# Performance work log

Hardware: AMD Instinct MI355X
Metric: run time of the kernel (lower is better)

Reference implementation:

```python
import jax, jax.numpy as jnp
from jax import lax
import numpy as np

B, T, F = 32, 512, 512
NUM_OUTPUTS = 23   # joints
DEV_CLASSES = 8
# layer specs: (input_dim, units)
LAYERS = [(F, 1024), (1024, 128), (128, NUM_OUTPUTS),
          (128 + NUM_OUTPUTS, 256), (256, 128), (128, DEV_CLASSES)]


def _gru_params(key, fan_in, units):
    k1, k2, k3 = jax.random.split(key, 3)
    kernel = jax.random.normal(k1, (fan_in, 3 * units), jnp.float32) / jnp.sqrt(jnp.float32(fan_in))
    rkernel = jax.random.normal(k2, (units, 3 * units), jnp.float32) * jnp.float32(0.02)
    bias = jnp.zeros((2, 3 * units), jnp.float32)  # [input_bias, recurrent_bias] (reset_after=True)
    return kernel, rkernel, bias


def setup_inputs() -> dict:
    key = jax.random.key(0)
    keys = jax.random.split(key, 7)
    inp = {"x": jax.random.normal(keys[0], (B, T, F), jnp.float32)}
    for i, (fi, u) in enumerate(LAYERS):
        k, r, b = _gru_params(keys[i + 1], fi, u)
        inp[f"k{i+1}"] = k
        inp[f"r{i+1}"] = r
        inp[f"b{i+1}"] = b
    return inp


def gru(x, kernel, rkernel, bias, act):
    """Keras GRU, reset_after=True, recurrent_activation=sigmoid, gate order z|r|h.
    x: [B,T,F]; kernel: [F,3U]; rkernel: [U,3U]; bias: [2,3U]. Returns [B,T,U]."""
    units = rkernel.shape[0]
    b_i, b_r = bias[0], bias[1]
    # precompute input projections for all timesteps (one big GEMM)
    xp = jnp.einsum('btf,fg->btg', x, kernel) + b_i  # [B,T,3U]

    def step(h, xt):
        rp = h @ rkernel + b_r                       # [B,3U]
        xz, xr, xh = jnp.split(xt, 3, axis=-1)
        rz, rr, rh = jnp.split(rp, 3, axis=-1)
        z = jax.nn.sigmoid(xz + rz)
        r = jax.nn.sigmoid(xr + rr)
        hh = act(xh + r * rh)                        # reset applied AFTER recurrent matmul
        h_new = z * h + (1.0 - z) * hh
        return h_new, h_new

    h0 = jnp.zeros((x.shape[0], units), x.dtype)
    _, ys = lax.scan(step, h0, jnp.swapaxes(xp, 0, 1))  # scan over time
    return jnp.swapaxes(ys, 0, 1)                        # [B,T,U]


relu = jax.nn.relu
linear = lambda v: v


def reference(x, k1, r1, b1, k2, r2, b2, k3, r3, b3,
              k4, r4, b4, k5, r5, b5, k6, r6, b6):
    z = gru(x, k1, r1, b1, relu)          # tcn_gru1: 1024
    z1 = gru(z, k2, r2, b2, relu)         # tcn_gru2: 128
    ye = gru(z1, k3, r3, b3, linear)      # tcn_dgru: num_outputs
    yc = jnp.concatenate([z1, ye], axis=-1)
    y = gru(yc, k4, r4, b4, relu)         # dev_gru1: 256
    y = gru(y, k5, r5, b5, relu)          # dev_gru2: 128
    yd = gru(y, k6, r6, b6, linear)       # dev_dgru: dev_classes
    return ye, yd
```

## Files before the change

### kernel.cpp

```cpp
#include <hip/hip_runtime.h>
#include <hip/hip_bf16.h>
#include <cstdint>
#include <cstddef>

#define BB 32
#define TT 512

typedef short s8v __attribute__((ext_vector_type(8)));
typedef float f4v __attribute__((ext_vector_type(4)));
typedef unsigned long long u64;
typedef unsigned short u16;
typedef unsigned int u32;

__device__ __forceinline__ short f2b(float x) {
  __hip_bfloat16 h = __float2bfloat16(x);
  return *reinterpret_cast<short*>(&h);
}
__device__ __forceinline__ float b2f(u16 x) {
  __hip_bfloat16 h = *reinterpret_cast<__hip_bfloat16*>(&x);
  return __bfloat162float(h);
}
__device__ __forceinline__ float sigm(float x) { return 1.f / (1.f + __expf(-x)); }

__device__ __forceinline__ f4v load16_sc(const void* p) {
  f4v v;
  asm volatile("global_load_dwordx4 %0, %1, off sc0 sc1" : "=v"(v) : "v"(p));
  return v;
}
__device__ __forceinline__ void vm_wait0() {
  asm volatile("s_waitcnt vmcnt(0)" ::: "memory");
}
__device__ __forceinline__ u32 ldP(const u32* p) {
  return __hip_atomic_load(p, __ATOMIC_RELAXED, __HIP_MEMORY_SCOPE_AGENT);
}
__device__ __forceinline__ void stW(u32* p, u32 v) {
  __hip_atomic_store(p, v, __ATOMIC_RELAXED, __HIP_MEMORY_SCOPE_AGENT);
}
__device__ __forceinline__ u32 ldW(const u32* p) {
  return __hip_atomic_load(p, __ATOMIC_RELAXED, __HIP_MEMORY_SCOPE_AGENT);
}

__device__ __forceinline__ void waitP(u32* flags, int baseA, int na, u32 thA,
                                      int baseB, int nbb, u32 thB,
                                      int baseS, int ns, u32 thS) {
  const int tid = threadIdx.x;
  for (;;) {
    int ok = 1;
    if (tid < na) ok = (ldP(&flags[(baseA + tid) * 32]) >= thA) ? 1 : 0;
    else if (tid < na + nbb) ok = (ldP(&flags[(baseB + tid - na) * 32]) >= thB) ? 1 : 0;
    else if (tid < na + nbb + ns) ok = (ldP(&flags[(baseS + tid - na - nbb) * 32]) >= thS) ? 1 : 0;
    if (__syncthreads_count(ok) == (int)blockDim.x) break;
    __builtin_amdgcn_s_sleep(1);
  }
}

__global__ __launch_bounds__(256) void cast_bf16(const float* __restrict__ in,
                                                 u16* __restrict__ outp, int n4) {
  int i = blockIdx.x * 256 + threadIdx.x;
  if (i < n4) {
    float4 v = *(const float4*)(in + (size_t)i * 4);
    u16 o[4] = {(u16)f2b(v.x), (u16)f2b(v.y), (u16)f2b(v.z), (u16)f2b(v.w)};
    *(u64*)(outp + (size_t)i * 4) = *(const u64*)o;
  }
}

__global__ __launch_bounds__(256) void prep_frags(const float* __restrict__ src,
                                                  u16* __restrict__ dst,
                                                  int N, int Ksrc, int Ks,
                                                  int JT, int U, int recmode, int total_fid) {
  int t = blockIdx.x * 256 + threadIdx.x;
  int lane = t & 63, fid = t >> 6;
  if (fid >= total_fid) return;
  int l15 = lane & 15, quad = lane >> 4;
  int ks = fid % Ks;
  int n, valid_n;
  if (recmode) {
    int rest = fid / Ks;
    int jt = rest % JT;
    int g = rest / JT;
    int jj = jt * 16 + l15;
    n = g * U + jj;
    valid_n = (jj < U) ? 1 : 0;
  } else {
    int nt = fid / Ks;
    n = nt * 16 + l15;
    valid_n = (n < N) ? 1 : 0;
  }
  u16* o = dst + ((size_t)fid * 64 + lane) * 8;
#pragma unroll
  for (int j = 0; j < 8; ++j) {
    int k = ks * 32 + quad * 8 + j;
    float v = (valid_n && k < Ksrc) ? src[(size_t)k * N + n] : 0.f;
    o[j] = (u16)f2b(v);
  }
}

__global__ __launch_bounds__(256) void prep_comb(const float* __restrict__ Kmat,
                                                 const float* __restrict__ Rmat,
                                                 u16* __restrict__ dst,
                                                 int N, int U, int w1v, int w1p,
                                                 int w2v, int w2p, int Ks, int JT,
                                                 int total_fid) {
  int t = blockIdx.x * 256 + threadIdx.x;
  int lane = t & 63, fid = t >> 6;
  if (fid >= total_fid) return;
  int l15 = lane & 15, quad = lane >> 4;
  int ks = fid % Ks;
  int rest = fid / Ks;
  int jt = rest % JT;
  int g = rest / JT;
  int j = jt * 16 + l15;
  bool jv = (j < U);
  int n = g * U + (jv ? j : 0);
  u16* o = dst + ((size_t)fid * 64 + lane) * 8;
#pragma unroll
  for (int jj = 0; jj < 8; ++jj) {
    int k = ks * 32 + quad * 8 + jj;
    float v = 0.f;
    if (jv) {
      if (k < w1p) {
        if (k < w1v) v = Kmat[(size_t)k * N + n];
      } else if (k < w1p + w2p) {
        int kr = k - w1p;
        if (kr < w2v) v = Kmat[(size_t)(w1v + kr) * N + n];
      } else {
        int rr = k - w1p - w2p;
        if (rr < U) v = Rmat[(size_t)rr * N + n];
      }
    }
    o[jj] = (u16)f2b(v);
  }
}

__global__ __launch_bounds__(256) void gemm_mfma(const u16* __restrict__ A, int strideA, int Kact,
                                                 const u16* __restrict__ Bf,
                                                 const float* __restrict__ bias,
                                                 float* __restrict__ C,
                                                 int N, int Ntiles, int Ks,
                                                 int t0, int tcLog2) {
  __shared__ char sha[16 * 2056];
  const int tid = threadIdx.x;
  const int lane = tid & 63, l15 = lane & 15, quad = lane >> 4, w = tid >> 6;
  const int KS4 = Ks * 8;
  const int rowB = Ks * 64 + 8;
  const int bm = blockIdx.y * 16;

  for (int i = tid; i < 16 * KS4; i += 256) {
    int r = i / KS4, u = i - r * KS4;
    u64 v = 0;
    if (u * 4 < Kact) {
      int rl = bm + r;
      size_t grow;
      if (t0 >= 0) {
        int tcm = (1 << tcLog2) - 1;
        grow = (((size_t)(rl >> tcLog2)) << 9) + t0 + (rl & tcm);
      } else {
        grow = (size_t)rl;
      }
      v = *((const u64*)(A + grow * (size_t)strideA) + u);
    }
    *(u64*)(sha + r * rowB + u * 8) = v;
  }
  __syncthreads();

  f4v acc[4];
  f4v z4 = {0.f, 0.f, 0.f, 0.f};
#pragma unroll
  for (int q = 0; q < 4; ++q) acc[q] = z4;

  const int ntb = blockIdx.x * 16 + w * 4;
  for (int ks = 0; ks < Ks; ++ks) {
    int off = l15 * rowB + ks * 64 + quad * 16;
    s8v a = *(const s8v*)(sha + off);
#pragma unroll
    for (int q = 0; q < 4; ++q) {
      int nt = ntb + q;
      if (nt < Ntiles) {
        s8v b = *(const s8v*)(Bf + (((size_t)nt * Ks + ks) * 64 + lane) * 8);
        acc[q] = __builtin_amdgcn_mfma_f32_16x16x32_bf16(a, b, acc[q], 0, 0, 0);
      }
    }
  }
#pragma unroll
  for (int q = 0; q < 4; ++q) {
    int nt = ntb + q;
    if (nt >= Ntiles) continue;
    int col = nt * 16 + l15;
    if (col < N) {
      float bv = bias[col];
#pragma unroll
      for (int r = 0; r < 4; ++r) {
        int rowl = bm + quad * 4 + r;
        C[(size_t)rowl * N + col] = acc[q][r] + bv;
      }
    }
  }
}

struct GCfg {
  const u16 *s1, *s2;
  const u16* Bf;
  const float* bias;
  u16* ydst;
  float* fdst;
  u16* hglob;
  int w1p, w2p, Upad, U, Ks, ksIn, JT, nb, base, act, wfd;
  int baseA, na, baseB, nbb;
};

#define SMEM_BYTES 91648
#define HPOFF 74240

__device__ __attribute__((noinline)) void stage_l1(
    const float* xp, const u16* Bf, const float* brec, u16* hbuf, u16* yout,
    u32* flags, int t0, int tc, char* smem) {
  const int tid = threadIdx.x;
  const int lane = tid & 63, l15 = lane & 15, quad = (lane >> 4) & 3;
  const int w = tid >> 6;
  const int blk = blockIdx.x;
  const bool work = (w < 4);
  const int jt = blk * 4 + (w & 3);
  const int j = jt * 16 + l15;
  const int HP = 32 * 1024;

  const float bz = brec[j], brr = brec[1024 + j], bh = brec[2048 + j];
  float hprev[8];
  if (work) {
    const u32* hp = (const u32*)(hbuf + (size_t)(t0 & 1) * HP);
#pragma unroll
    for (int Mt = 0; Mt < 2; ++Mt)
#pragma unroll
      for (int r = 0; r < 4; ++r) {
        int b = Mt * 16 + quad * 4 + r;
        u32 wd = ldW(hp + ((b * 1024 + (j & ~1)) >> 1));
        hprev[Mt * 4 + r] = b2f((j & 1) ? (u16)(wd >> 16) : (u16)(wd & 0xffff));
      }
  }

  for (int tt = 0; tt < tc; ++tt) {
    const int t = t0 + tt;
    waitP(flags, 0, 16, (u32)t, 0, 0, 0, 0, 0, 0);
    float xv[3][8];
    if (work) {
#pragma unroll
      for (int Mt = 0; Mt < 2; ++Mt)
#pragma unroll
        for (int r = 0; r < 4; ++r) {
          int b = Mt * 16 + quad * 4 + r;
          const float* xr_ = xp + ((size_t)b * tc + tt) * 3072;
          xv[0][Mt * 4 + r] = __builtin_nontemporal_load(xr_ + j);
          xv[1][Mt * 4 + r] = __builtin_nontemporal_load(xr_ + 1024 + j);
          xv[2][Mt * 4 + r] = __builtin_nontemporal_load(xr_ + 2048 + j);
        }
    }
    {
      const char* hsrc = (const char*)(hbuf + (size_t)(t & 1) * HP);
      f4v vals[8];
#pragma unroll
      for (int i = 0; i < 8; ++i)
        vals[i] = load16_sc(hsrc + (size_t)(tid + i * 512) * 16);
      vm_wait0();
#pragma unroll
      for (int i = 0; i < 8; ++i) {
        int g16 = tid + i * 512;
        *(f4v*)(smem + (g16 >> 7) * 2064 + (g16 & 127) * 16) = vals[i];
      }
    }
    __syncthreads();
    f4v acc[3][2];
    f4v z4 = {0.f, 0.f, 0.f, 0.f};
#pragma unroll
    for (int g = 0; g < 3; ++g) { acc[g][0] = z4; acc[g][1] = z4; }
    if (work) {
#pragma unroll 4
      for (int ks = 0; ks < 32; ++ks) {
        s8v a0 = *(const s8v*)(smem + l15 * 2064 + ks * 64 + quad * 16);
        s8v a1 = *(const s8v*)(smem + (16 + l15) * 2064 + ks * 64 + quad * 16);
#pragma unroll
        for (int g = 0; g < 3; ++g) {
          s8v b = *(const s8v*)(Bf + (((size_t)(g * 64 + jt) * 32 + ks) * 64 + lane) * 8);
          acc[g][0] = __builtin_amdgcn_mfma_f32_16x16x32_bf16(a0, b, acc[g][0], 0, 0, 0);
          acc[g][1] = __builtin_amdgcn_mfma_f32_16x16x32_bf16(a1, b, acc[g][1], 0, 0, 0);
        }
      }
      u16* hdst = hbuf + (size_t)((t + 1) & 1) * HP;
#pragma unroll
      for (int Mt = 0; Mt < 2; ++Mt)
#pragma unroll
        for (int r = 0; r < 4; ++r) {
          int b = Mt * 16 + quad * 4 + r;
          size_t row = (size_t)b * tc + tt;
          float z = sigm(xv[0][Mt * 4 + r] + acc[0][Mt][r] + bz);
          float rr = sigm(xv[1][Mt * 4 + r] + acc[1][Mt][r] + brr);
          float hh = fmaxf(xv[2][Mt * 4 + r] + rr * (acc[2][Mt][r] + bh), 0.f);
          float hnew = z * hprev[Mt * 4 + r] + (1.f - z) * hh;
          hprev[Mt * 4 + r] = hnew;
          float part = __shfl_xor(hnew, 1, 64);
          if ((l15 & 1) == 0) {
            u32 wd = (u32)(u16)f2b(hnew) | ((u32)(u16)f2b(part) << 16);
            stW((u32*)hdst + ((b * 1024 + j) >> 1), wd);
            stW((u32*)yout + ((row * 1024 + j) >> 1), wd);
          }
        }
    }
    __syncthreads();
    if (tid == 0) stW(&flags[blk * 32], (u32)(t + 1));
  }
}

__device__ __attribute__((noinline)) void stage_gen(
    const GCfg& c, int bs, u32* flags, int t0, int tc, int initH, char* smem) {
  const int tid = threadIdx.x;
  const int lane = tid & 63, l15 = lane & 15, quad = (lane >> 4) & 3;
  const int w = tid >> 6;
  const int rowA = (c.w1p + c.w2p + c.Upad) * 2 + 16;
  const int rowH = c.Upad * 2 + 16;
  char* Ab = smem;
  char* Hp = smem + HPOFF;
  const int HB = 32 * rowH;
  const int uIn = (c.w1p + c.w2p) >> 3;
  const int uH = c.Upad >> 3;
  const int upr = uIn + ((c.nb > 1) ? uH : 0);
  const int total_units = 32 * upr;
  const int u1 = c.w1p >> 3;
  const int U = c.U;
  const int HPstride = 32 * c.Upad;

  int tjt[2];
  bool tv[2];
#pragma unroll
  for (int i = 0; i < 2; ++i) {
    int jt = (w + i * 8) * c.nb + bs;
    tv[i] = (jt < c.JT);
    tjt[i] = tv[i] ? jt : 0;
  }

  const float* b0 = c.bias;
  const float* b1 = c.bias + 3 * U;
  float bz[2], br_[2], bih[2], brh[2];
  int jl[2];
  bool jv[2];
#pragma unroll
  for (int i = 0; i < 2; ++i) {
    int j = tjt[i] * 16 + l15;
    jv[i] = tv[i] && (j < U);
    int jc = jv[i] ? j : 0;
    jl[i] = j;
    bz[i] = b0[jc] + b1[jc];
    br_[i] = b0[U + jc] + b1[U + jc];
    bih[i] = b0[2 * U + jc];
    brh[i] = b1[2 * U + jc];
  }

  if (c.nb == 1) {
    for (int i = tid; i < (2 * HB) >> 2; i += 512) ((u32*)Hp)[i] = 0;
    __syncthreads();
    if (!initH) {
      for (int i = tid; i < 32 * uH; i += 512) {
        int m = i / uH, u = i - m * uH;
        *(f4v*)(Hp + (t0 & 1) * HB + m * rowH + u * 16) = *((const f4v*)c.hglob + i);
      }
    }
    __syncthreads();
  }

  float hprev[2][8];
#pragma unroll
  for (int i = 0; i < 2; ++i) {
    if (!tv[i]) continue;
#pragma unroll
    for (int Mt = 0; Mt < 2; ++Mt)
#pragma unroll
      for (int r = 0; r < 4; ++r) {
        int b = Mt * 16 + quad * 4 + r;
        float hv;
        if (c.nb > 1) {
          u32 wd = ldW((const u32*)c.hglob + (((t0 & 1) * HPstride + b * c.Upad + (jl[i] & ~1)) >> 1));
          hv = b2f((jl[i] & 1) ? (u16)(wd >> 16) : (u16)(wd & 0xffff));
        } else {
          hv = b2f(*(const u16*)(Hp + (t0 & 1) * HB + b * rowH + jl[i] * 2));
        }
        hprev[i][Mt * 4 + r] = jv[i] ? hv : 0.f;
      }
  }

  for (int tt = 0; tt < tc; ++tt) {
    const int t = t0 + tt;
    waitP(flags, c.baseA, c.na, (u32)(t + 1), c.baseB, c.nbb, (u32)(t + 1),
          c.base, (c.nb > 1) ? c.nb : 0, (u32)t);
    {
      f4v vals[10];
      int offs[10];
#pragma unroll
      for (int i = 0; i < 10; ++i) {
        int idx = tid + i * 512;
        int pidx = (idx < total_units) ? idx : (total_units - 1);
        int m = pidx / upr, u = pidx - m * upr;
        const char* src;
        if (u < u1)
          src = (const char*)c.s1 + ((size_t)(m * tc + tt) * c.w1p + (u << 3)) * 2;
        else if (u < uIn)
          src = (const char*)c.s2 + ((size_t)(m * tc + tt) * c.w2p + ((u - u1) << 3)) * 2;
        else
          src = (const char*)c.hglob + ((size_t)(t & 1) * HPstride + m * c.Upad + ((u - uIn) << 3)) * 2;
        vals[i] = load16_sc(src);
        offs[i] = m * rowA + u * 16;
      }
      vm_wait0();
#pragma unroll
      for (int i = 0; i < 10; ++i)
        if (tid + i * 512 < total_units) *(f4v*)(Ab + offs[i]) = vals[i];
    }
    __syncthreads();
    f4v az[2][2], ar[2][2], axh[2][2], arh[2][2];
    f4v z4 = {0.f, 0.f, 0.f, 0.f};
#pragma unroll
    for (int i = 0; i < 2; ++i)
#pragma unroll
      for (int Mt = 0; Mt < 2; ++Mt) { az[i][Mt] = z4; ar[i][Mt] = z4; axh[i][Mt] = z4; arh[i][Mt] = z4; }
    for (int ks = 0; ks < c.ksIn; ++ks) {
      s8v aM[2];
#pragma unroll
      for (int Mt = 0; Mt < 2; ++Mt)
        aM[Mt] = *(const s8v*)(Ab + (Mt * 16 + l15) * rowA + ks * 64 + quad * 16);
#pragma unroll
      for (int i = 0; i < 2; ++i) {
        if (!tv[i]) break;
        const u16* bb = c.Bf + ((size_t)tjt[i] * c.Ks + ks) * 512 + lane * 8;
        s8v bz_ = *(const s8v*)(bb);
        s8v br2 = *(const s8v*)(bb + (size_t)c.JT * c.Ks * 512);
        s8v bh2 = *(const s8v*)(bb + (size_t)2 * c.JT * c.Ks * 512);
#pragma unroll
        for (int Mt = 0; Mt < 2; ++Mt) {
          az[i][Mt] = __builtin_amdgcn_mfma_f32_16x16x32_bf16(aM[Mt], bz_, az[i][Mt], 0, 0, 0);
          ar[i][Mt] = __builtin_amdgcn_mfma_f32_16x16x32_bf16(aM[Mt], br2, ar[i][Mt], 0, 0, 0);
          axh[i][Mt] = __builtin_amdgcn_mfma_f32_16x16x32_bf16(aM[Mt], bh2, axh[i][Mt], 0, 0, 0);
        }
      }
    }
    for (int ks = c.ksIn; ks < c.Ks; ++ks) {
      s8v aM[2];
#pragma unroll
      for (int Mt = 0; Mt < 2; ++Mt) {
        if (c.nb > 1)
          aM[Mt] = *(const s8v*)(Ab + (Mt * 16 + l15) * rowA + ks * 64 + quad * 16);
        else
          aM[Mt] = *(const s8v*)(Hp + (t & 1) * HB + (Mt * 16 + l15) * rowH + (ks - c.ksIn) * 64 + quad * 16);
      }
#pragma unroll
      for (int i = 0; i < 2; ++i) {
        if (!tv[i]) break;
        const u16* bb = c.Bf + ((size_t)tjt[i] * c.Ks + ks) * 512 + lane * 8;
        s8v bz_ = *(const s8v*)(bb);
        s8v br2 = *(const s8v*)(bb + (size_t)c.JT * c.Ks * 512);
        s8v bh2 = *(const s8v*)(bb + (size_t)2 * c.JT * c.Ks * 512);
#pragma unroll
        for (int Mt = 0; Mt < 2; ++Mt) {
          az[i][Mt] = __builtin_amdgcn_mfma_f32_16x16x32_bf16(aM[Mt], bz_, az[i][Mt], 0, 0, 0);
          ar[i][Mt] = __builtin_amdgcn_mfma_f32_16x16x32_bf16(aM[Mt], br2, ar[i][Mt], 0, 0, 0);
          arh[i][Mt] = __builtin_amdgcn_mfma_f32_16x16x32_bf16(aM[Mt], bh2, arh[i][Mt], 0, 0, 0);
        }
      }
    }
#pragma unroll
    for (int i = 0; i < 2; ++i) {
      if (!tv[i]) break;
#pragma unroll
      for (int Mt = 0; Mt < 2; ++Mt)
#pragma unroll
        for (int r = 0; r < 4; ++r) {
          int b = Mt * 16 + quad * 4 + r;
          size_t row = (size_t)b * tc + tt;
          float z = sigm(az[i][Mt][r] + bz[i]);
          float rg = sigm(ar[i][Mt][r] + br_[i]);
          float hh = axh[i][Mt][r] + bih[i] + rg * (arh[i][Mt][r] + brh[i]);
          if (c.act) hh = fmaxf(hh, 0.f);
          float hnew = z * hprev[i][Mt * 4 + r] + (1.f - z) * hh;
          if (!jv[i]) hnew = 0.f;
          hprev[i][Mt * 4 + r] = hnew;
          int j = jl[i];
          float part = __shfl_xor(hnew, 1, 64);
          u32 wd = (u32)(u16)f2b(hnew) | ((u32)(u16)f2b(part) << 16);
          if ((l15 & 1) == 0) {
            if (c.ydst) stW((u32*)c.ydst + ((row * c.Upad + j) >> 1), wd);
            if (c.nb > 1)
              stW((u32*)c.hglob + ((((t + 1) & 1) * HPstride + b * c.Upad + j) >> 1), wd);
          }
          if (c.nb == 1) *(u16*)(Hp + ((t + 1) & 1) * HB + b * rowH + j * 2) = (u16)f2b(hnew);
          if (c.fdst && jv[i] && j < c.wfd)
            c.fdst[((size_t)b * TT + t) * c.wfd + j] = hnew;
        }
    }
    __syncthreads();
    if (tid == 0) stW(&flags[(c.base + bs) * 32], (u32)(t + 1));
  }
  if (c.nb == 1) {
    int pf = (t0 + tc) & 1;
    for (int i = tid; i < 32 * uH; i += 512) {
      int m = i / uH, u = i - m * uH;
      *((f4v*)c.hglob + i) = *(const f4v*)(Hp + pf * HB + m * rowH + u * 16);
    }
  }
}

__global__ __launch_bounds__(512, 1) void pipeline(
    const float* xp, const u16* BfL1, const float* brecL1, u16* hbufL1, u16* y1c,
    GCfg c1, GCfg c2, GCfg c3, GCfg c4, GCfg c5,
    u32* flags, int t0, int tc, int initH) {
  __shared__ char smem[SMEM_BYTES];
  int blk = blockIdx.x;
  if (blk < 16) stage_l1(xp, BfL1, brecL1, hbufL1, y1c, flags, t0, tc, smem);
  else if (blk < 18) stage_gen(c1, blk - 16, flags, t0, tc, initH, smem);
  else if (blk < 19) stage_gen(c2, 0, flags, t0, tc, initH, smem);
  else if (blk < 21) stage_gen(c3, blk - 19, flags, t0, tc, initH, smem);
  else if (blk < 22) stage_gen(c4, 0, flags, t0, tc, initH, smem);
  else stage_gen(c5, 0, flags, t0, tc, initH, smem);
}

extern "C" void kernel_launch(void* const* d_in, const int* in_sizes, int n_in,
                              void* d_out, int out_size, void* d_ws, size_t ws_size,
                              hipStream_t stream) {
  const float* x = (const float*)d_in[0];

  int tcLog2 = 6;
  {
    size_t fixed = (size_t)16384 * 512 * 2
                   + (3145728ull + 1572864ull + 442368 + 15360 + 319488 + 147456 + 7680) * 2
                   + 300000;
    for (; tcLog2 >= 4; --tcLog2) {
      size_t rc = (size_t)BB << tcLog2;
      size_t per = rc * 3072 * 4 + rc * (1024 + 128 + 32 + 256 + 128) * 2 + 8192;
      if (fixed + per <= ws_size || tcLog2 == 4) break;
    }
  }
  const int Tc = 1 << tcLog2;
  const int NCk = TT / Tc;
  const size_t RC = (size_t)BB * Tc;

  char* ws = (char*)d_ws;
  size_t off = 0;
  auto alloc = [&](size_t bytes) -> char* {
    char* p = ws + off;
    off += (bytes + 255) & ~(size_t)255;
    return p;
  };

  u32* flags = (u32*)alloc(23 * 32 * sizeof(u32));
  u16* hbufL1 = (u16*)alloc((size_t)2 * 32 * 1024 * 2);
  u16* hb2 = (u16*)alloc((size_t)2 * 32 * 128 * 2);
  u16* hb4 = (u16*)alloc((size_t)2 * 32 * 256 * 2);
  u16* hs3 = (u16*)alloc((size_t)32 * 32 * 2);
  u16* hs5 = (u16*)alloc((size_t)32 * 128 * 2);
  u16* hs6 = (u16*)alloc((size_t)32 * 32 * 2);
  u16* recB1 = (u16*)alloc(3145728ull * 2);
  u16* gemB1 = (u16*)alloc(1572864ull * 2);
  u16* cB[5];
  const size_t cBe[5] = {442368, 15360, 319488, 147456, 7680};
  for (int i = 0; i < 5; ++i) cB[i] = (u16*)alloc(cBe[i] * 2);
  u16* x16 = (u16*)alloc((size_t)16384 * 512 * 2);
  float* xp = (float*)alloc(RC * 3072 * sizeof(float));
  u16* y1c = (u16*)alloc(RC * 1024 * 2);
  u16* y2c = (u16*)alloc(RC * 128 * 2);
  u16* yec = (u16*)alloc(RC * 32 * 2);
  u16* y4c = (u16*)alloc(RC * 256 * 2);
  u16* y5c = (u16*)alloc(RC * 128 * 2);

  float* outye = (float*)d_out;
  float* outyd = outye + (size_t)BB * TT * 23;

  hipMemsetAsync(flags, 0, 23 * 32 * sizeof(u32), stream);
  hipMemsetAsync(hbufL1, 0, (size_t)2 * 32 * 1024 * 2, stream);
  hipMemsetAsync(hb2, 0, (size_t)2 * 32 * 128 * 2, stream);
  hipMemsetAsync(hb4, 0, (size_t)2 * 32 * 256 * 2, stream);

  {
    int n4 = (16384 * 512) / 4;
    hipLaunchKernelGGL(cast_bf16, dim3((n4 + 255) / 256), dim3(256), 0, stream, x, x16, n4);
    hipLaunchKernelGGL(prep_frags, dim3((3 * 64 * 32 * 64 + 255) / 256), dim3(256), 0, stream,
                       (const float*)d_in[2], recB1, 3072, 1024, 32, 64, 1024, 1, 3 * 64 * 32);
    hipLaunchKernelGGL(prep_frags, dim3((192 * 16 * 64 + 255) / 256), dim3(256), 0, stream,
                       (const float*)d_in[1], gemB1, 3072, 512, 16, 0, 0, 0, 192 * 16);
    const int pc[5][8] = {
        {384, 128, 1024, 1024, 0, 0, 36, 8},
        {69, 23, 128, 128, 0, 0, 5, 2},
        {768, 256, 128, 128, 23, 32, 13, 16},
        {384, 128, 256, 256, 0, 0, 12, 8},
        {24, 8, 128, 128, 0, 0, 5, 1}};
    for (int i = 0; i < 5; ++i) {
      int l = i + 1;
      int tf = 3 * pc[i][7] * pc[i][6];
      hipLaunchKernelGGL(prep_comb, dim3((tf * 64 + 255) / 256), dim3(256), 0, stream,
                         (const float*)d_in[1 + 3 * l], (const float*)d_in[2 + 3 * l], cB[i],
                         pc[i][0], pc[i][1], pc[i][2], pc[i][3], pc[i][4], pc[i][5],
                         pc[i][6], pc[i][7], tf);
    }
  }

  GCfg c1 = {y1c, nullptr, cB[0], (const float*)d_in[6], y2c, nullptr, hb2,
             1024, 0, 128, 128, 36, 32, 8, 2, 16, 1, 0, 0, 16, 0, 0};
  GCfg c2 = {y2c, nullptr, cB[1], (const float*)d_in[9], yec, outye, hs3,
             128, 0, 32, 23, 5, 4, 2, 1, 18, 0, 23, 16, 2, 0, 0};
  GCfg c3 = {y2c, yec, cB[2], (const float*)d_in[12], y4c, nullptr, hb4,
             128, 32, 256, 256, 13, 5, 16, 2, 19, 1, 0, 16, 2, 18, 1};
  GCfg c4 = {y4c, nullptr, cB[3], (const float*)d_in[15], y5c, nullptr, hs5,
             256, 0, 128, 128, 12, 8, 8, 1, 21, 1, 0, 19, 2, 0, 0};
  GCfg c5 = {y5c, nullptr, cB[4], (const float*)d_in[18], nullptr, outyd, hs6,
             128, 0, 32, 8, 5, 4, 1, 1, 22, 0, 8, 21, 1, 0, 0};

  const float* biasL1 = (const float*)d_in[3];

  for (int c = 0; c < NCk; ++c) {
    const int t0 = c * Tc;
    hipLaunchKernelGGL(gemm_mfma, dim3(12, (unsigned)(RC / 16)), dim3(256), 0, stream,
                       x16, 512, 512, gemB1, biasL1, xp, 3072, 192, 16, t0, tcLog2);
    hipLaunchKernelGGL(pipeline, dim3(23), dim3(512), 0, stream,
                       xp, recB1, biasL1 + 3072, hbufL1, y1c,
                       c1, c2, c3, c4, c5, flags, t0, Tc, (c == 0) ? 1 : 0);
  }
}
```

Before: 16.32 ms.

## Use per-wave flags, double-buffered LDS, and x prefetch in layer-1 GRU

```diff
diff --git a/kernel.cpp b/kernel.cpp
--- a/kernel.cpp
+++ b/kernel.cpp
@@ -40,16 +40,16 @@
   return __hip_atomic_load(p, __ATOMIC_RELAXED, __HIP_MEMORY_SCOPE_AGENT);
 }
 
-__device__ __forceinline__ void waitP(u32* flags, int baseA, int na, u32 thA,
+__device__ __forceinline__ void waitW(u32* flags, int baseA, int na, u32 thA,
                                       int baseB, int nbb, u32 thB,
                                       int baseS, int ns, u32 thS) {
-  const int tid = threadIdx.x;
+  const int lane = threadIdx.x & 63;
   for (;;) {
-    int ok = 1;
-    if (tid < na) ok = (ldP(&flags[(baseA + tid) * 32]) >= thA) ? 1 : 0;
-    else if (tid < na + nbb) ok = (ldP(&flags[(baseB + tid - na) * 32]) >= thB) ? 1 : 0;
-    else if (tid < na + nbb + ns) ok = (ldP(&flags[(baseS + tid - na - nbb) * 32]) >= thS) ? 1 : 0;
-    if (__syncthreads_count(ok) == (int)blockDim.x) break;
+    bool ok = true;
+    if (lane < na) ok = (ldP(&flags[(baseA + lane) * 32]) >= thA);
+    if (nbb && lane < nbb) ok = ok && (ldP(&flags[(baseB + lane) * 32]) >= thB);
+    if (ns && lane < ns) ok = ok && (ldP(&flags[(baseS + lane) * 32]) >= thS);
+    if (__all(ok)) break;
     __builtin_amdgcn_s_sleep(1);
   }
 }
@@ -208,7 +208,8 @@
   int baseA, na, baseB, nbb;
 };
 
-#define SMEM_BYTES 91648
+#define SMEM_BYTES 132096
+#define HBUF1 66048
 #define HPOFF 74240
 
 __device__ __attribute__((noinline)) void stage_l1(
@@ -222,6 +223,7 @@
   const int jt = blk * 4 + (w & 3);
   const int j = jt * 16 + l15;
   const int HP = 32 * 1024;
+  const int slot = blk * 4 + (w & 3);
 
   const float bz = brec[j], brr = brec[1024 + j], bh = brec[2048 + j];
   float hprev[8];
@@ -237,22 +239,24 @@
       }
   }
 
+  float xc[3][8];
+  if (work) {
+#pragma unroll
+    for (int Mt = 0; Mt < 2; ++Mt)
+#pragma unroll
+      for (int r = 0; r < 4; ++r) {
+        int b = Mt * 16 + quad * 4 + r;
+        const float* xr_ = xp + ((size_t)b * tc + 0) * 3072;
+        xc[0][Mt * 4 + r] = __builtin_nontemporal_load(xr_ + j);
+        xc[1][Mt * 4 + r] = __builtin_nontemporal_load(xr_ + 1024 + j);
+        xc[2][Mt * 4 + r] = __builtin_nontemporal_load(xr_ + 2048 + j);
+      }
+  }
+
   for (int tt = 0; tt < tc; ++tt) {
     const int t = t0 + tt;
-    waitP(flags, 0, 16, (u32)t, 0, 0, 0, 0, 0, 0);
-    float xv[3][8];
-    if (work) {
-#pragma unroll
-      for (int Mt = 0; Mt < 2; ++Mt)
-#pragma unroll
-        for (int r = 0; r < 4; ++r) {
-          int b = Mt * 16 + quad * 4 + r;
-          const float* xr_ = xp + ((size_t)b * tc + tt) * 3072;
-          xv[0][Mt * 4 + r] = __builtin_nontemporal_load(xr_ + j);
-          xv[1][Mt * 4 + r] = __builtin_nontemporal_load(xr_ + 1024 + j);
-          xv[2][Mt * 4 + r] = __builtin_nontemporal_load(xr_ + 2048 + j);
-        }
-    }
+    waitW(flags, 0, 64, (u32)t, 0, 0, 0, 0, 0, 0);
+    char* buf = smem + (t & 1) * HBUF1;
     {
       const char* hsrc = (const char*)(hbuf + (size_t)(t & 1) * HP);
       f4v vals[8];
@@ -263,19 +267,33 @@
 #pragma unroll
       for (int i = 0; i < 8; ++i) {
         int g16 = tid + i * 512;
-        *(f4v*)(smem + (g16 >> 7) * 2064 + (g16 & 127) * 16) = vals[i];
+        *(f4v*)(buf + (g16 >> 7) * 2064 + (g16 & 127) * 16) = vals[i];
       }
     }
     __syncthreads();
-    f4v acc[3][2];
-    f4v z4 = {0.f, 0.f, 0.f, 0.f};
-#pragma unroll
-    for (int g = 0; g < 3; ++g) { acc[g][0] = z4; acc[g][1] = z4; }
+    float xn[3][8];
     if (work) {
+      int ttn = (tt + 1 < tc) ? tt + 1 : tt;
+#pragma unroll
+      for (int Mt = 0; Mt < 2; ++Mt)
+#pragma unroll
+        for (int r = 0; r < 4; ++r) {
+          int b = Mt * 16 + quad * 4 + r;
+          const float* xr_ = xp + ((size_t)b * tc + ttn) * 3072;
+          xn[0][Mt * 4 + r] = __builtin_nontemporal_load(xr_ + j);
+          xn[1][Mt * 4 + r] = __builtin_nontemporal_load(xr_ + 1024 + j);
+          xn[2][Mt * 4 + r] = __builtin_nontemporal_load(xr_ + 2048 + j);
+        }
+    }
+    if (work) {
+      f4v acc[3][2];
+      f4v z4 = {0.f, 0.f, 0.f, 0.f};
+#pragma unroll
+      for (int g = 0; g < 3; ++g) { acc[g][0] = z4; acc[g][1] = z4; }
 #pragma unroll 4
       for (int ks = 0; ks < 32; ++ks) {
-        s8v a0 = *(const s8v*)(smem + l15 * 2064 + ks * 64 + quad * 16);
-        s8v a1 = *(const s8v*)(smem + (16 + l15) * 2064 + ks * 64 + quad * 16);
+        s8v a0 = *(const s8v*)(buf + l15 * 2064 + ks * 64 + quad * 16);
+        s8v a1 = *(const s8v*)(buf + (16 + l15) * 2064 + ks * 64 + quad * 16);
 #pragma unroll
         for (int g = 0; g < 3; ++g) {
           s8v b = *(const s8v*)(Bf + (((size_t)(g * 64 + jt) * 32 + ks) * 64 + lane) * 8);
@@ -290,9 +308,9 @@
         for (int r = 0; r < 4; ++r) {
           int b = Mt * 16 + quad * 4 + r;
           size_t row = (size_t)b * tc + tt;
-          float z = sigm(xv[0][Mt * 4 + r] + acc[0][Mt][r] + bz);
-          float rr = sigm(xv[1][Mt * 4 + r] + acc[1][Mt][r] + brr);
-          float hh = fmaxf(xv[2][Mt * 4 + r] + rr * (acc[2][Mt][r] + bh), 0.f);
+          float z = sigm(xc[0][Mt * 4 + r] + acc[0][Mt][r] + bz);
+          float rr = sigm(xc[1][Mt * 4 + r] + acc[1][Mt][r] + brr);
+          float hh = fmaxf(xc[2][Mt * 4 + r] + rr * (acc[2][Mt][r] + bh), 0.f);
           float hnew = z * hprev[Mt * 4 + r] + (1.f - z) * hh;
           hprev[Mt * 4 + r] = hnew;
           float part = __shfl_xor(hnew, 1, 64);
@@ -302,9 +320,13 @@
             stW((u32*)yout + ((row * 1024 + j) >> 1), wd);
           }
         }
-    }
-    __syncthreads();
-    if (tid == 0) stW(&flags[blk * 32], (u32)(t + 1));
+      vm_wait0();
+      if (lane == 0) stW(&flags[slot * 32], (u32)(t + 1));
+#pragma unroll
+      for (int g = 0; g < 3; ++g)
+#pragma unroll
+        for (int i = 0; i < 8; ++i) xc[g][i] = xn[g][i];
+    }
   }
 }
 
@@ -386,7 +408,7 @@
 
   for (int tt = 0; tt < tc; ++tt) {
     const int t = t0 + tt;
-    waitP(flags, c.baseA, c.na, (u32)(t + 1), c.baseB, c.nbb, (u32)(t + 1),
+    waitW(flags, c.baseA, c.na, (u32)(t + 1), c.baseB, c.nbb, (u32)(t + 1),
           c.base, (c.nb > 1) ? c.nb : 0, (u32)t);
     {
       f4v vals[10];
@@ -545,7 +567,7 @@
     return p;
   };
 
-  u32* flags = (u32*)alloc(23 * 32 * sizeof(u32));
+  u32* flags = (u32*)alloc(71 * 32 * sizeof(u32));
   u16* hbufL1 = (u16*)alloc((size_t)2 * 32 * 1024 * 2);
   u16* hb2 = (u16*)alloc((size_t)2 * 32 * 128 * 2);
   u16* hb4 = (u16*)alloc((size_t)2 * 32 * 256 * 2);
@@ -568,7 +590,7 @@
   float* outye = (float*)d_out;
   float* outyd = outye + (size_t)BB * TT * 23;
 
-  hipMemsetAsync(flags, 0, 23 * 32 * sizeof(u32), stream);
+  hipMemsetAsync(flags, 0, 71 * 32 * sizeof(u32), stream);
   hipMemsetAsync(hbufL1, 0, (size_t)2 * 32 * 1024 * 2, stream);
   hipMemsetAsync(hb2, 0, (size_t)2 * 32 * 128 * 2, stream);
   hipMemsetAsync(hb4, 0, (size_t)2 * 32 * 256 * 2, stream);
@@ -597,15 +619,15 @@
   }
 
   GCfg c1 = {y1c, nullptr, cB[0], (const float*)d_in[6], y2c, nullptr, hb2,
-             1024, 0, 128, 128, 36, 32, 8, 2, 16, 1, 0, 0, 16, 0, 0};
+             1024, 0, 128, 128, 36, 32, 8, 2, 64, 1, 0, 0, 64, 0, 0};
   GCfg c2 = {y2c, nullptr, cB[1], (const float*)d_in[9], yec, outye, hs3,
-             128, 0, 32, 23, 5, 4, 2, 1, 18, 0, 23, 16, 2, 0, 0};
+             128, 0, 32, 23, 5, 4, 2, 1, 66, 0, 23, 64, 2, 0, 0};
   GCfg c3 = {y2c, yec, cB[2], (const float*)d_in[12], y4c, nullptr, hb4,
-             128, 32, 256, 256, 13, 5, 16, 2, 19, 1, 0, 16, 2, 18, 1};
+             128, 32, 256, 256, 13, 5, 16, 2, 67, 1, 0, 64, 2, 66, 1};
   GCfg c4 = {y4c, nullptr, cB[3], (const float*)d_in[15], y5c, nullptr, hs5,
-             256, 0, 128, 128, 12, 8, 8, 1, 21, 1, 0, 19, 2, 0, 0};
+             256, 0, 128, 128, 12, 8, 8, 1, 69, 1, 0, 67, 2, 0, 0};
   GCfg c5 = {y5c, nullptr, cB[4], (const float*)d_in[18], nullptr, outyd, hs6,
-             128, 0, 32, 8, 5, 4, 1, 1, 22, 0, 8, 21, 1, 0, 0};
+             128, 0, 32, 8, 5, 4, 1, 1, 70, 0, 8, 69, 1, 0, 0};
 
   const float* biasL1 = (const float*)d_in[3];
 
```

Measured after the change: 16.31 ms. No clear change (-0.1%).
